# Optimization experiments

Hardware: AMD Instinct MI355X
Metric: run time of the kernel (lower is better)

Reference implementation:

```python
import jax, jax.numpy as jnp
import numpy as np

B = 256; NROIS = 200; IN = 200; HID = 128; L = 4; H = 8; RATIO = 0.5
K = int(np.ceil(RATIO * NROIS))        # SAGPooling top-k per graph = 100
N = B * NROIS                          # total nodes = 51200
DEG = 32; EPG = NROIS * DEG; E_EDGES = B * EPG  # 1,638,400 edges
EMB = HID * L                          # MHA embed dim = 512
DH = EMB // H

def _xavier(k, shape):
    fan_in, fan_out = shape[-2], shape[-1]
    lim = float(np.sqrt(6.0 / (fan_in + fan_out)))
    return jax.random.uniform(k, shape, jnp.float32, -lim, lim)

def setup_inputs() -> dict:
    key = jax.random.key(0)
    ks = jax.random.split(key, 16)
    x = jax.random.normal(ks[0], (N, IN), jnp.float32)
    # block-diagonal edge list: edges stay within each graph's node range
    src = jax.random.randint(ks[1], (E_EDGES,), 0, NROIS, jnp.int32)
    dst = jax.random.randint(ks[2], (E_EDGES,), 0, NROIS, jnp.int32)
    off = jnp.repeat(jnp.arange(B, dtype=jnp.int32) * NROIS, EPG)
    edge_index = jnp.stack([src + off, dst + off])
    edge_attr = jax.random.normal(ks[3], (E_EDGES,), jnp.float32)  # unused by the math
    batch = jnp.repeat(jnp.arange(B, dtype=jnp.int32), NROIS)
    return dict(
        x=x, edge_index=edge_index, edge_attr=edge_attr, batch=batch,
        gcn_w0=_xavier(ks[4], (IN, HID)),
        gcn_w=_xavier(ks[5], (L - 1, HID, HID)),
        gcn_b=jnp.zeros((L, HID), jnp.float32),
        lin1_w0=_xavier(ks[6], (IN + HID, HID)),
        lin1_w=_xavier(ks[7], (L - 1, 2 * HID, HID)),
        lin1_b=jnp.zeros((L, HID), jnp.float32),
        lin2_w=_xavier(ks[8], (L, HID, HID)),
        lin2_b=jnp.zeros((L, HID), jnp.float32),
        sag_w1=_xavier(ks[9], (HID, 1)),
        sag_w2=_xavier(ks[10], (HID, 1)),
        sag_b=jnp.zeros((1,), jnp.float32),
        mha_in_w=_xavier(ks[11], (3 * EMB, EMB)),
        mha_in_b=jnp.zeros((3 * EMB,), jnp.float32),
        mha_out_w=_xavier(ks[12], (EMB, EMB)),
        mha_out_b=jnp.zeros((EMB,), jnp.float32),
        fin_w=_xavier(ks[13], (EMB, HID)),
        fin_b=jnp.zeros((HID,), jnp.float32),
    )

def _gcn_conv(x, src, dst, W, b):
    xw = x @ W
    deg = jax.ops.segment_sum(jnp.ones_like(dst, jnp.float32), dst, num_segments=N) + 1.0
    dinv = jax.lax.rsqrt(deg)
    norm = dinv[src] * dinv[dst]                     # [E]
    agg = jax.ops.segment_sum(xw[src] * norm[:, None], dst, num_segments=N)
    agg = agg + xw * (dinv * dinv)[:, None]          # self-loop term
    return agg + b

def _gcblock(x, src, dst, gw, gb, l1w, l1b, l2w, l2b):
    x1 = jnp.tanh(_gcn_conv(x, src, dst, gw, gb))
    h = jnp.tanh(jnp.concatenate([x, x1], axis=1) @ l1w + l1b)
    return jnp.tanh(h @ l2w + l2b)

def _sag_pool_pad(z, src, dst, w1, w2, b):
    # SAGPooling score via PyG GraphConv (aggr='add'): lin_rel(sum_j x_j) + lin_root(x_i)
    neigh = jax.ops.segment_sum(z[src], dst, num_segments=N)
    score = (neigh @ w1)[:, 0] + b[0] + (z @ w2)[:, 0]        # [N]
    s3 = score.reshape(B, NROIS)
    vals, idx = jax.lax.top_k(s3, K)                           # [B,K]
    z3 = z.reshape(B, NROIS, HID)
    pooled = jnp.take_along_axis(z3, idx[:, :, None], axis=1) * jnp.tanh(vals)[:, :, None]
    zpad = jnp.zeros_like(z3).at[jnp.arange(B)[:, None], idx].set(pooled)
    return zpad.reshape(N, HID)

def reference(x, edge_index, edge_attr, batch,
              gcn_w0, gcn_w, gcn_b, lin1_w0, lin1_w, lin1_b, lin2_w, lin2_b,
              sag_w1, sag_w2, sag_b,
              mha_in_w, mha_in_b, mha_out_w, mha_out_b, fin_w, fin_b):
    src, dst = edge_index[0], edge_index[1]
    z = x
    pads = []
    for i in range(L):
        gw = gcn_w0 if i == 0 else gcn_w[i - 1]
        l1w = lin1_w0 if i == 0 else lin1_w[i - 1]
        z = _gcblock(z, src, dst, gw, gcn_b[i], l1w, lin1_b[i], lin2_w[i], lin2_b[i])
        pads.append(_sag_pool_pad(z, src, dst, sag_w1, sag_w2, sag_b))
    xc = jnp.concatenate(pads, axis=1).reshape(B, NROIS, EMB)   # [B,S,E]
    # MultiheadAttention (batch_first, eval mode -> no dropout)
    qkv = xc @ mha_in_w.T + mha_in_b                             # [B,S,3E]
    q, k, v = jnp.split(qkv, 3, axis=-1)
    def heads(t):
        return t.reshape(B, NROIS, H, DH).transpose(0, 2, 1, 3)  # [B,H,S,dh]
    q, k, v = heads(q), heads(k), heads(v)
    scores = jnp.einsum('bhqd,bhkd->bhqk', q, k) / np.sqrt(DH)
    attn = jax.nn.softmax(scores, axis=-1)                       # [B,H,S,S]
    o = jnp.einsum('bhqk,bhkd->bhqd', attn, v).transpose(0, 2, 1, 3).reshape(B, NROIS, EMB)
    o = o @ mha_out_w.T + mha_out_b
    attn_weights = attn.mean(axis=1)                             # avg over heads [B,S,S]
    # readout: global_mean_pool over each graph's nrois nodes
    pooled = o.mean(axis=1)                                      # [B,E]
    out = jnp.tanh(pooled @ fin_w + fin_b)                       # [B,HID]
    return out, attn_weights
```

## Files before the change

kernel.cpp:

```cpp
#include <hip/hip_runtime.h>
#include <hip/hip_fp16.h>


#define GB   256
#define SS   200
#define KIN  200
#define HD   128
#define NLAY 4
#define NHD  8
#define TOPK 100
#define NT   (GB * SS)
#define EPG_ 6400
#define NE_  (GB * EPG_)
#define EMB_ 512

typedef _Float16 half8 __attribute__((ext_vector_type(8)));
typedef _Float16 half4v __attribute__((ext_vector_type(4)));
typedef float floatx4 __attribute__((ext_vector_type(4)));

__global__ __launch_bounds__(256) void k_build_A(const int* __restrict__ src,
                                                 const int* __restrict__ dst,
                                                 float* __restrict__ A) {
  int e = blockIdx.x * 256 + threadIdx.x;
  if (e >= NE_) return;
  int d = dst[e], s = src[e];
  int b = d / SS;
  int dl = d - b * SS;
  int sl = s - b * SS;
  atomicAdd(&A[((size_t)b * SS + dl) * SS + sl], 1.0f);
}

__global__ __launch_bounds__(256) void k_dinv(const float* __restrict__ A,
                                              float* __restrict__ dinv) {
  int node = blockIdx.x * 4 + (threadIdx.x >> 6);
  int lane = threadIdx.x & 63;
  const float* r = A + (size_t)node * SS;
  float v = r[lane] + r[lane + 64] + r[lane + 128];
  if (lane < 8) v += r[lane + 192];
#pragma unroll
  for (int o = 32; o; o >>= 1) v += __shfl_xor(v, o);
  if (lane == 0) dinv[node] = rsqrtf(v + 1.0f);
}

__global__ __launch_bounds__(256) void k_prep_all(
    const float* __restrict__ gcn_w0, const float* __restrict__ gcn_w,
    const float* __restrict__ lin1_w0, const float* __restrict__ lin1_w,
    const float* __restrict__ lin2_w,
    __half* __restrict__ whi, __half* __restrict__ wlo) {
  const int mat = blockIdx.x >> 7;
  const int n   = blockIdx.x & 127;
  const int l = mat / 3, which = mat % 3;
  const float* src;
  int K, Kpad;
  if (which == 0) {
    K = l ? HD : KIN;  Kpad = l ? 128 : 256;
    src = l ? gcn_w + (size_t)(l - 1) * HD * HD : gcn_w0;
  } else if (which == 1) {
    K = l ? 2 * HD : KIN + HD;  Kpad = l ? 256 : 384;
    src = l ? lin1_w + (size_t)(l - 1) * 2 * HD * HD : lin1_w0;
  } else {
    K = HD;  Kpad = HD;
    src = lin2_w + (size_t)l * HD * HD;
  }
  int off = (l == 0) ? (which == 0 ? 0 : (which == 1 ? 32768 : 81920))
                     : 98304 + (l - 1) * 65536 +
                       (which == 0 ? 0 : (which == 1 ? 16384 : 49152));
  _Float16* wh = (_Float16*)whi + (size_t)off + (size_t)n * Kpad;
  _Float16* wl = (_Float16*)wlo + (size_t)off + (size_t)n * Kpad;
  for (int k = threadIdx.x; k < Kpad; k += 256) {
    float v = (k < K) ? src[(size_t)k * HD + n] : 0.f;
    _Float16 h = (_Float16)v;
    wh[k] = h;
    wl[k] = (_Float16)(v - (float)h);
  }
}

__global__ __launch_bounds__(256) void k_prep_w16(const float* __restrict__ W,
                                                  __half* __restrict__ W16) {
  int i = blockIdx.x * 256 + threadIdx.x;
  float4 v = reinterpret_cast<const float4*>(W)[i];
  half4v h = {(_Float16)v.x, (_Float16)v.y, (_Float16)v.z, (_Float16)v.w};
  *reinterpret_cast<half4v*>((_Float16*)W16 + (size_t)i * 4) = h;
}

__global__ __launch_bounds__(256) void k_node_mfma(
    const float* __restrict__ in1, int k1,
    const float* __restrict__ in2,
    const __half* __restrict__ Whi, const __half* __restrict__ Wlo,
    int Kpad,
    const float* __restrict__ bias,
    float* __restrict__ out, int doTanh) {
  const int m0 = blockIdx.x * 64;
  const int t = threadIdx.x;
  const int wave = t >> 6, lane = t & 63;
  const int col = lane & 15, quad = lane >> 4;
  const int wm = (wave & 1) * 32;
  const int wn = (wave >> 1) * 64;
  __shared__ __align__(16) _Float16 Ah[64][72];
  __shared__ __align__(16) _Float16 Al[64][72];
  floatx4 acc[2][4] = {};
  const int lr = t >> 2;
  const int lk = (t & 3) * 16;
  const _Float16* Wh = (const _Float16*)Whi;
  const _Float16* Wl = (const _Float16*)Wlo;

  for (int k0 = 0; k0 < Kpad; k0 += 64) {
    __syncthreads();
#pragma unroll
    for (int q = 0; q < 4; ++q) {
      int kg = k0 + lk + q * 4;
      float4 v = {0.f, 0.f, 0.f, 0.f};
      if (kg < k1)
        v = *reinterpret_cast<const float4*>(&in1[(size_t)(m0 + lr) * k1 + kg]);
      else if (in2 && kg < k1 + HD)
        v = *reinterpret_cast<const float4*>(&in2[(size_t)(m0 + lr) * HD + (kg - k1)]);
      half4v h = {(_Float16)v.x, (_Float16)v.y, (_Float16)v.z, (_Float16)v.w};
      half4v lo = {(_Float16)(v.x - (float)h.x), (_Float16)(v.y - (float)h.y),
                   (_Float16)(v.z - (float)h.z), (_Float16)(v.w - (float)h.w)};
      *reinterpret_cast<half4v*>(&Ah[lr][lk + q * 4]) = h;
      *reinterpret_cast<half4v*>(&Al[lr][lk + q * 4]) = lo;
    }
    __syncthreads();
#pragma unroll
    for (int ks = 0; ks < 2; ++ks) {
      half8 ah[2], al[2], bh[4], bl[4];
#pragma unroll
      for (int i = 0; i < 2; ++i) {
        ah[i] = *reinterpret_cast<const half8*>(&Ah[wm + i * 16 + col][ks * 32 + quad * 8]);
        al[i] = *reinterpret_cast<const half8*>(&Al[wm + i * 16 + col][ks * 32 + quad * 8]);
      }
#pragma unroll
      for (int j = 0; j < 4; ++j) {
        const size_t wo = (size_t)(wn + j * 16 + col) * Kpad + k0 + ks * 32 + quad * 8;
        bh[j] = *reinterpret_cast<const half8*>(Wh + wo);
        bl[j] = *reinterpret_cast<const half8*>(Wl + wo);
      }
#pragma unroll
      for (int i = 0; i < 2; ++i)
#pragma unroll
        for (int j = 0; j < 4; ++j) {
          acc[i][j] = __builtin_amdgcn_mfma_f32_16x16x32_f16(ah[i], bh[j], acc[i][j], 0, 0, 0);
          acc[i][j] = __builtin_amdgcn_mfma_f32_16x16x32_f16(ah[i], bl[j], acc[i][j], 0, 0, 0);
          acc[i][j] = __builtin_amdgcn_mfma_f32_16x16x32_f16(al[i], bh[j], acc[i][j], 0, 0, 0);
        }
    }
  }
#pragma unroll
  for (int j = 0; j < 4; ++j) {
    int n = wn + j * 16 + col;
    float bb = bias ? bias[n] : 0.f;
#pragma unroll
    for (int i = 0; i < 2; ++i) {
      int rbase = m0 + wm + i * 16 + quad * 4;
#pragma unroll
      for (int r = 0; r < 4; ++r) {
        float v = acc[i][j][r] + bb;
        if (doTanh) v = tanhf(v);
        out[(size_t)(rbase + r) * HD + n] = v;
      }
    }
  }
}

__global__ __launch_bounds__(256) void k_agg_mfma(
    const float* __restrict__ A, const float* __restrict__ dinv,
    const float* __restrict__ xw, const float* __restrict__ bias,
    float* __restrict__ out) {
  const int b    = blockIdx.x >> 1;
  const int row0 = (blockIdx.x & 1) * 128;
  const int t = threadIdx.x;
  const int wave = t >> 6, lane = t & 63;
  const int col = lane & 15, quad = lane >> 4;
  const int wm = (wave & 1) * 64, wn = (wave >> 1) * 64;
  __shared__ __align__(16) _Float16 Ah[128][72];
  __shared__ __align__(16) _Float16 Al[128][72];
  __shared__ __align__(16) _Float16 Bh[128][72];
  __shared__ __align__(16) _Float16 Bl[128][72];
  __shared__ float dvs[256];
  dvs[t] = (t < SS) ? dinv[b * SS + t] : 0.f;
  floatx4 acc[4][4] = {};
  const float* Ab  = A  + (size_t)b * SS * SS;
  const float* xwb = xw + (size_t)b * SS * HD;
  const int lr = t >> 1, lk = (t & 1) * 32;
  const int d = row0 + lr;
  __syncthreads();
  const float dvd = (d < SS) ? dvs[d] : 0.f;

  for (int k0 = 0; k0 < 256; k0 += 64) {
    __syncthreads();
#pragma unroll
    for (int q = 0; q < 8; ++q) {
      int s = k0 + lk + q * 4;
      float4 v = {0.f, 0.f, 0.f, 0.f};
      if (d < SS && s < SS)
        v = *reinterpret_cast<const float4*>(&Ab[(size_t)d * SS + s]);
      float e0 = (v.x + ((s + 0 == d) ? 1.f : 0.f)) * dvd * dvs[(s + 0) & 255];
      float e1 = (v.y + ((s + 1 == d) ? 1.f : 0.f)) * dvd * dvs[(s + 1) & 255];
      float e2 = (v.z + ((s + 2 == d) ? 1.f : 0.f)) * dvd * dvs[(s + 2) & 255];
      float e3 = (v.w + ((s + 3 == d) ? 1.f : 0.f)) * dvd * dvs[(s + 3) & 255];
      half4v h = {(_Float16)e0, (_Float16)e1, (_Float16)e2, (_Float16)e3};
      half4v lo = {(_Float16)(e0 - (float)h.x), (_Float16)(e1 - (float)h.y),
                   (_Float16)(e2 - (float)h.z), (_Float16)(e3 - (float)h.w)};
      *reinterpret_cast<half4v*>(&Ah[lr][lk + q * 4]) = h;
      *reinterpret_cast<half4v*>(&Al[lr][lk + q * 4]) = lo;
    }
#pragma unroll
    for (int p = 0; p < 8; ++p) {
      int idx = t + p * 256;
      int c4 = idx & 31, ss = idx >> 5;
      int s = k0 + ss;
      float4 v = {0.f, 0.f, 0.f, 0.f};
      if (s < SS)
        v = *reinterpret_cast<const float4*>(&xwb[(size_t)s * HD + c4 * 4]);
      int ssx = ss ^ ((c4 & 7) << 3);
      float e[4] = {v.x, v.y, v.z, v.w};
#pragma unroll
      for (int j = 0; j < 4; ++j) {
        _Float16 h = (_Float16)e[j];
        Bh[c4 * 4 + j][ssx] = h;
        Bl[c4 * 4 + j][ssx] = (_Float16)(e[j] - (float)h);
      }
    }
    __syncthreads();
#pragma unroll
    for (int ks = 0; ks < 2; ++ks) {
      half8 ah[4], al[4], bh[4], bl[4];
#pragma unroll
      for (int i = 0; i < 4; ++i) {
        ah[i] = *reinterpret_cast<const half8*>(&Ah[wm + i * 16 + col][ks * 32 + quad * 8]);
        al[i] = *reinterpret_cast<const half8*>(&Al[wm + i * 16 + col][ks * 32 + quad * 8]);
      }
#pragma unroll
      for (int j = 0; j < 4; ++j) {
        int n = wn + j * 16 + col;
        int koff = (ks * 32 + quad * 8) ^ (((n >> 2) & 7) << 3);
        bh[j] = *reinterpret_cast<const half8*>(&Bh[n][koff]);
        bl[j] = *reinterpret_cast<const half8*>(&Bl[n][koff]);
      }
#pragma unroll
      for (int i = 0; i < 4; ++i)
#pragma unroll
        for (int j = 0; j < 4; ++j) {
          acc[i][j] = __builtin_amdgcn_mfma_f32_16x16x32_f16(ah[i], bh[j], acc[i][j], 0, 0, 0);
          acc[i][j] = __builtin_amdgcn_mfma_f32_16x16x32_f16(ah[i], bl[j], acc[i][j], 0, 0, 0);
          acc[i][j] = __builtin_amdgcn_mfma_f32_16x16x32_f16(al[i], bh[j], acc[i][j], 0, 0, 0);
        }
    }
  }
#pragma unroll
  for (int j = 0; j < 4; ++j) {
    int n = wn + j * 16 + col;
    float bb = bias[n];
#pragma unroll
    for (int i = 0; i < 4; ++i) {
      int rbase = row0 + wm + i * 16 + quad * 4;
#pragma unroll
      for (int r = 0; r < 4; ++r) {
        int row = rbase + r;
        if (row < SS)
          out[((size_t)b * SS + row) * HD + n] = tanhf(acc[i][j][r] + bb);
      }
    }
  }
}

__global__ __launch_bounds__(256) void k_sag(
    const float* __restrict__ z, const float* __restrict__ A,
    const float* __restrict__ w1, const float* __restrict__ w2,
    const float* __restrict__ sb,
    __half* __restrict__ xch, __half* __restrict__ xcl, int layer) {
  const int b = blockIdx.x, t = threadIdx.x;
  __shared__ float w1s[HD], w2s[HD];
  __shared__ float zw1[SS], sc[SS], fac[SS];
  if (t < HD) { w1s[t] = w1[t]; w2s[t] = w2[t]; }
  __syncthreads();
  float a2 = 0.f;
  if (t < SS) {
    const float4* zr = reinterpret_cast<const float4*>(&z[((size_t)b * SS + t) * HD]);
    float a1 = 0.f;
#pragma unroll
    for (int q = 0; q < HD / 4; ++q) {
      float4 v = zr[q];
      a1 += v.x * w1s[4 * q] + v.y * w1s[4 * q + 1] + v.z * w1s[4 * q + 2] + v.w * w1s[4 * q + 3];
      a2 += v.x * w2s[4 * q] + v.y * w2s[4 * q + 1] + v.z * w2s[4 * q + 2] + v.w * w2s[4 * q + 3];
    }
    zw1[t] = a1;
  }
  __syncthreads();
  if (t < SS) {
    float s = sb[0] + a2;
    const float4* ar = reinterpret_cast<const float4*>(&A[((size_t)b * SS + t) * SS]);
#pragma unroll 5
    for (int q = 0; q < SS / 4; ++q) {
      float4 v = ar[q];
      s += v.x * zw1[4 * q] + v.y * zw1[4 * q + 1] + v.z * zw1[4 * q + 2] + v.w * zw1[4 * q + 3];
    }
    sc[t] = s;
  }
  __syncthreads();
  if (t < SS) {
    float si = sc[t];
    int cnt = 0;
    for (int j = 0; j < SS; ++j) {
      float sj = sc[j];
      cnt += (sj > si || (sj == si && j < t)) ? 1 : 0;
    }
    fac[t] = (cnt < TOPK) ? tanhf(si) : 0.f;
  }
  __syncthreads();
  _Float16* xh = (_Float16*)xch;
  _Float16* xl = (_Float16*)xcl;
  for (int idx = t; idx < SS * HD; idx += 256) {
    int row = idx >> 7, c = idx & 127;
    float v = fac[row] * z[((size_t)b * SS + row) * HD + c];
    _Float16 h = (_Float16)v;
    size_t o = ((size_t)b * SS + row) * EMB_ + layer * HD + c;
    xh[o] = h;
    xl[o] = (_Float16)(v - (float)h);
  }
}

__global__ __launch_bounds__(256) void k_proj(
    const __half* __restrict__ xch, const __half* __restrict__ Win16,
    const float* __restrict__ bin, __half* __restrict__ QKh) {
  const int wg = (blockIdx.x & 7) * 400 + (blockIdx.x >> 3);
  const int bm = wg >> 3;
  const int bn = wg & 7;
  const int m0 = bm * 128, n0 = bn * 128;
  const int t = threadIdx.x;
  const int wave = t >> 6, lane = t & 63;
  const int col = lane & 15, quad = lane >> 4;
  const int wm = (wave & 1) * 64;
  const int wn = (wave >> 1) * 64;
  floatx4 acc[4][4] = {};
  const _Float16* X = (const _Float16*)xch;
  const _Float16* W = (const _Float16*)Win16;
  const _Float16* xa[4];
  const _Float16* wb[4];
#pragma unroll
  for (int i = 0; i < 4; ++i)
    xa[i] = X + (size_t)(m0 + wm + i * 16 + col) * EMB_ + quad * 8;
#pragma unroll
  for (int j = 0; j < 4; ++j)
    wb[j] = W + (size_t)(n0 + wn + j * 16 + col) * EMB_ + quad * 8;

#pragma unroll 4
  for (int k0 = 0; k0 < EMB_; k0 += 32) {
    half8 af[4], bf[4];
#pragma unroll
    for (int i = 0; i < 4; ++i) af[i] = *reinterpret_cast<const half8*>(xa[i] + k0);
#pragma unroll
    for (int j = 0; j < 4; ++j) bf[j] = *reinterpret_cast<const half8*>(wb[j] + k0);
#pragma unroll
    for (int i = 0; i < 4; ++i)
#pragma unroll
      for (int j = 0; j < 4; ++j)
        acc[i][j] = __builtin_amdgcn_mfma_f32_16x16x32_f16(af[i], bf[j], acc[i][j], 0, 0, 0);
  }
#pragma unroll
  for (int j = 0; j < 4; ++j) {
    int c = n0 + wn + j * 16 + col;
    float bb = bin[c];
#pragma unroll
    for (int i = 0; i < 4; ++i) {
      int rbase = m0 + wm + i * 16 + quad * 4;
#pragma unroll
      for (int r = 0; r < 4; ++r)
        QKh[(size_t)(rbase + r) * 1024 + c] = __float2half(acc[i][j][r] + bb);
    }
  }
}

__global__ __launch_bounds__(256) void k_attn(
    const __half* __restrict__ QKh,
    float* __restrict__ cpbuf,
    float* __restrict__ attn) {
  const int bx = (blockIdx.x & 7) * 416 + (blockIdx.x >> 3);
  const int b  = bx / 13;
  const int it = bx % 13;
  const int i0 = it * 16;
  const int rows = (SS - i0 >= 16) ? 16 : (SS - i0);
  const int t    = threadIdx.x;
  const int wave = t >> 6;
  const int lane = t & 63;
  const int col  = lane & 15;
  const int quad = lane >> 4;

  __shared__ __align__(16) float Ss[16][212];

  float am[13];
  int   soff[13];
  int   kmax = 0;
#pragma unroll
  for (int k = 0; k < 13; ++k) {
    int idx = t + (k << 8);
    am[k] = 0.f;
    if (idx < rows * 200) {
      int i = idx / 200;
      soff[k] = idx + 12 * i;
      kmax = k + 1;
    } else soff[k] = 0;
  }

  const _Float16* Qbase = (const _Float16*)QKh + (size_t)b * SS * 1024;
  const _Float16* qrow = Qbase + (size_t)(i0 + col) * 1024 + quad * 8;
  const _Float16* krow[4];
#pragma unroll
  for (int m = 0; m < 4; ++m) {
    int jt = wave + m * 4;
    krow[m] = Qbase + (size_t)(jt * 16 + col) * 1024 + 512 + quad * 8;
  }

  for (int h = 0; h < NHD; ++h) {
    const int hoff = h * 64;
    half8 a0 = *reinterpret_cast<const half8*>(qrow + hoff);
    half8 a1 = *reinterpret_cast<const half8*>(qrow + hoff + 32);
#pragma unroll
    for (int m = 0; m < 4; ++m) {
      int jt = wave + m * 4;
      if (jt < 13) {
        half8 b0 = *reinterpret_cast<const half8*>(krow[m] + hoff);
        half8 b1 = *reinterpret_cast<const half8*>(krow[m] + hoff + 32);
        floatx4 acc = {0.f, 0.f, 0.f, 0.f};
        acc = __builtin_amdgcn_mfma_f32_16x16x32_f16(a0, b0, acc, 0, 0, 0);
        acc = __builtin_amdgcn_mfma_f32_16x16x32_f16(a1, b1, acc, 0, 0, 0);
#pragma unroll
        for (int r = 0; r < 4; ++r)
          Ss[quad * 4 + r][jt * 16 + col] = acc[r] * 0.125f;
      }
    }
    __syncthreads();
#pragma unroll
    for (int ri = 0; ri < 4; ++ri) {
      int r = wave * 4 + ri;
      if (r < rows) {
        float* srow = &Ss[r][0];
        float s0 = srow[lane], s1 = srow[lane + 64], s2 = srow[lane + 128];
        float s3 = (lane < 8) ? srow[lane + 192] : -1e30f;
        float mx = fmaxf(fmaxf(s0, s1), fmaxf(s2, s3));
#pragma unroll
        for (int o = 32; o; o >>= 1) mx = fmaxf(mx, __shfl_xor(mx, o));
        float e0 = __expf(s0 - mx), e1 = __expf(s1 - mx), e2 = __expf(s2 - mx);
        float e3 = (lane < 8) ? __expf(s3 - mx) : 0.f;
        float sum = e0 + e1 + e2 + e3;
#pragma unroll
        for (int o = 32; o; o >>= 1) sum += __shfl_xor(sum, o);
        float rl = 1.0f / sum;
        srow[lane] = e0 * rl; srow[lane + 64] = e1 * rl; srow[lane + 128] = e2 * rl;
        if (lane < 8) srow[lane + 192] = e3 * rl;
      }
    }
    __syncthreads();
    const float* sflat = &Ss[0][0];
#pragma unroll
    for (int k = 0; k < 13; ++k)
      if (k < kmax) am[k] += sflat[soff[k]] * 0.125f;
    if (t < SS) {
      float s = 0.f;
      for (int i = 0; i < rows; ++i) s += Ss[i][t];
      atomicAdd(&cpbuf[((size_t)b * NHD + h) * SS + t], s);
    }
    __syncthreads();
  }
  float* abase = &attn[((size_t)b * SS + i0) * SS];
#pragma unroll
  for (int k = 0; k < 13; ++k)
    if (k < kmax) abase[t + (k << 8)] = am[k];
}

__global__ __launch_bounds__(256) void k_pool(
    const __half* __restrict__ xch, const __half* __restrict__ xcl,
    const float* __restrict__ cpbuf,
    const float* __restrict__ Win, const float* __restrict__ bin,
    float* __restrict__ pooled) {
  const int b = blockIdx.x, t = threadIdx.x;
  __shared__ float cps[NHD][SS];
  __shared__ float tvs[NHD][EMB_];
  for (int idx = t; idx < NHD * SS; idx += 256) {
    int h = idx / SS, j = idx - h * SS;
    cps[h][j] = cpbuf[((size_t)b * NHD + h) * SS + j];
  }
  __syncthreads();
  const _Float16* xh = (const _Float16*)xch + (size_t)b * SS * EMB_;
  const _Float16* xl = (const _Float16*)xcl + (size_t)b * SS * EMB_;
  float a0[NHD] = {0.f}, a1[NHD] = {0.f};
  for (int j = 0; j < SS; ++j) {
    float x0 = (float)xh[(size_t)j * EMB_ + t] + (float)xl[(size_t)j * EMB_ + t];
    float x1 = (float)xh[(size_t)j * EMB_ + t + 256] + (float)xl[(size_t)j * EMB_ + t + 256];
#pragma unroll
    for (int h = 0; h < NHD; ++h) {
      float c = cps[h][j];
      a0[h] += c * x0; a1[h] += c * x1;
    }
  }
#pragma unroll
  for (int h = 0; h < NHD; ++h) { tvs[h][t] = a0[h]; tvs[h][t + 256] = a1[h]; }
  __syncthreads();
  const int wv = t >> 6, lane = t & 63;
  for (int e = wv; e < EMB_; e += 4) {
    int h = e >> 6;
    const float* wr = Win + (size_t)(2 * EMB_ + e) * EMB_;
    float s = 0.f;
#pragma unroll
    for (int q = 0; q < 8; ++q) s += wr[lane + q * 64] * tvs[h][lane + q * 64];
#pragma unroll
    for (int o = 32; o; o >>= 1) s += __shfl_xor(s, o);
    if (lane == 0) pooled[(size_t)b * EMB_ + e] = bin[2 * EMB_ + e] * (float)SS + s;
  }
}

__global__ __launch_bounds__(256) void k_final(
    const float* __restrict__ pooled, const float* __restrict__ Wout,
    const float* __restrict__ bout, const float* __restrict__ finw,
    const float* __restrict__ finb, float* __restrict__ out) {
  const int b = blockIdx.x, t = threadIdx.x;
  __shared__ float pl[EMB_], po[EMB_];
  for (int k = t; k < EMB_; k += 256) pl[k] = pooled[(size_t)b * EMB_ + k] * (1.0f / (float)SS);
  __syncthreads();
  for (int e = t; e < EMB_; e += 256) {
    const float* wr = &Wout[(size_t)e * EMB_];
    float a = bout[e];
    for (int k = 0; k < EMB_; ++k) a += wr[k] * pl[k];
    po[e] = a;
  }
  __syncthreads();
  if (t < HD) {
    float a = finb[t];
    for (int e = 0; e < EMB_; ++e) a += po[e] * finw[(size_t)e * HD + t];
    out[(size_t)b * HD + t] = tanhf(a);
  }
}

extern "C" void kernel_launch(void* const* d_in, const int* in_sizes, int n_in,
                              void* d_out, int out_size, void* d_ws, size_t ws_size,
                              hipStream_t stream) {
  const float* x         = (const float*)d_in[0];
  const int*   ei        = (const int*)d_in[1];
  const float* gcn_w0    = (const float*)d_in[4];
  const float* gcn_w     = (const float*)d_in[5];
  const float* gcn_b     = (const float*)d_in[6];
  const float* lin1_w0   = (const float*)d_in[7];
  const float* lin1_w    = (const float*)d_in[8];
  const float* lin1_b    = (const float*)d_in[9];
  const float* lin2_w    = (const float*)d_in[10];
  const float* lin2_b    = (const float*)d_in[11];
  const float* sag_w1    = (const float*)d_in[12];
  const float* sag_w2    = (const float*)d_in[13];
  const float* sag_b     = (const float*)d_in[14];
  const float* mha_in_w  = (const float*)d_in[15];
  const float* mha_in_b  = (const float*)d_in[16];
  const float* mha_out_w = (const float*)d_in[17];
  const float* mha_out_b = (const float*)d_in[18];
  const float* fin_w     = (const float*)d_in[19];
  const float* fin_b     = (const float*)d_in[20];

  float* ws     = (float*)d_ws;
  float* dinv   = ws;
  float* Araw   = dinv + NT;
  float* buf0   = Araw + (size_t)GB * SS * SS;
  float* buf1   = buf0 + (size_t)NT * HD;
  float* zbuf   = buf1 + (size_t)NT * HD;
  float* xcf    = zbuf + (size_t)NT * HD;
  __half* xch   = (__half*)xcf;
  __half* xcl   = xch + (size_t)NT * EMB_;
  float* pooled = xcf + (size_t)NT * EMB_;
  __half* QKh  = (__half*)Araw;
  float* cpbuf = Araw + 26214400;

  float* outp = (float*)d_out;
  float* attn = outp + (size_t)GB * HD;

  __half* whi   = (__half*)attn;
  __half* wlo   = whi + 294912;
  __half* Win16 = wlo + 294912;

  hipMemsetAsync(Araw, 0, (size_t)GB * SS * SS * sizeof(float), stream);

  k_prep_all<<<12 * 128, 256, 0, stream>>>(gcn_w0, gcn_w, lin1_w0, lin1_w, lin2_w, whi, wlo);
  k_prep_w16<<<512, 256, 0, stream>>>(mha_in_w, Win16);
  k_build_A<<<NE_ / 256, 256, 0, stream>>>(ei, ei + NE_, Araw);
  k_dinv<<<NT / 4, 256, 0, stream>>>(Araw, dinv);

  static const int KPg[4]  = {256, 128, 128, 128};
  static const int KP1[4]  = {384, 256, 256, 256};
  static const int OFFg[4] = {0, 98304, 163840, 229376};
  static const int OFF1[4] = {32768, 114688, 180224, 245760};
  static const int OFF2[4] = {81920, 147456, 212992, 278528};

  for (int l = 0; l < NLAY; ++l) {
    const float* zin = (l == 0) ? x : zbuf;
    int k1 = (l == 0) ? KIN : HD;
    k_node_mfma<<<NT / 64, 256, 0, stream>>>(zin, k1, nullptr,
                                             whi + OFFg[l], wlo + OFFg[l], KPg[l],
                                             nullptr, buf0, 0);
    k_agg_mfma<<<GB * 2, 256, 0, stream>>>(Araw, dinv, buf0, gcn_b + l * HD, buf1);
    k_node_mfma<<<NT / 64, 256, 0, stream>>>(zin, k1, buf1,
                                             whi + OFF1[l], wlo + OFF1[l], KP1[l],
                                             lin1_b + l * HD, buf0, 1);
    k_node_mfma<<<NT / 64, 256, 0, stream>>>(buf0, HD, nullptr,
                                             whi + OFF2[l], wlo + OFF2[l], HD,
                                             lin2_b + l * HD, zbuf, 1);
    k_sag<<<GB, 256, 0, stream>>>(zbuf, Araw, sag_w1, sag_w2, sag_b, xch, xcl, l);
  }

  hipMemsetAsync(cpbuf, 0, (size_t)GB * NHD * SS * sizeof(float), stream);
  k_proj<<<(NT / 128) * 8, 256, 0, stream>>>(xch, Win16, mha_in_b, QKh);
  k_attn<<<GB * 13, 256, 0, stream>>>(QKh, cpbuf, attn);
  k_pool<<<GB, 256, 0, stream>>>(xch, xcl, cpbuf, mha_in_w, mha_in_b, pooled);
  k_final<<<GB, 256, 0, stream>>>(pooled, mha_out_w, mha_out_b, fin_w, fin_b, outp);
}
```

Measured before the change: 1.575 ms.

## Stage QKV projection tiles in LDS via direct global-to-LDS loads with swizzle

The QK projection GEMM previously had each wave load its MFMA fragments straight from global memory, so the same A and B rows were fetched redundantly across waves. Each block now stages 128x64 half tiles of A and B in shared memory using global_load_lds with an XOR swizzle, then reads fragments from LDS. This is meant to cut global traffic and improve coalescing, at the cost of two barriers per k-step and no double buffering.

Measured after the change: 1.450 ms. -7.9%, faster.

```diff
diff --git a/kernel.cpp b/kernel.cpp
--- a/kernel.cpp
+++ b/kernel.cpp
@@ -332,30 +332,51 @@
   const int col = lane & 15, quad = lane >> 4;
   const int wm = (wave & 1) * 64;
   const int wn = (wave >> 1) * 64;
+  __shared__ __align__(16) _Float16 As[128][64];
+  __shared__ __align__(16) _Float16 Bs[128][64];
   floatx4 acc[4][4] = {};
   const _Float16* X = (const _Float16*)xch;
   const _Float16* W = (const _Float16*)Win16;
-  const _Float16* xa[4];
-  const _Float16* wb[4];
-#pragma unroll
-  for (int i = 0; i < 4; ++i)
-    xa[i] = X + (size_t)(m0 + wm + i * 16 + col) * EMB_ + quad * 8;
-#pragma unroll
-  for (int j = 0; j < 4; ++j)
-    wb[j] = W + (size_t)(n0 + wn + j * 16 + col) * EMB_ + quad * 8;
-
-#pragma unroll 4
-  for (int k0 = 0; k0 < EMB_; k0 += 32) {
-    half8 af[4], bf[4];
-#pragma unroll
-    for (int i = 0; i < 4; ++i) af[i] = *reinterpret_cast<const half8*>(xa[i] + k0);
-#pragma unroll
-    for (int j = 0; j < 4; ++j) bf[j] = *reinterpret_cast<const half8*>(wb[j] + k0);
-#pragma unroll
-    for (int i = 0; i < 4; ++i)
+
+  const int srow = lane >> 3;
+  const int sch  = (lane & 7) ^ srow;
+  const int arow = wave * 8 + srow;
+  const int fsw = col & 7;
+
+  for (int k0 = 0; k0 < EMB_; k0 += 64) {
+#pragma unroll
+    for (int q = 0; q < 4; ++q) {
+      const _Float16* ga = X + (size_t)(m0 + q * 32 + arow) * EMB_ + k0 + sch * 8;
+      __builtin_amdgcn_global_load_lds(
+          (const __attribute__((address_space(1))) void*)ga,
+          (__attribute__((address_space(3))) void*)((char*)&As[0][0] + q * 4096 + wave * 1024),
+          16, 0, 0);
+      const _Float16* gb = W + (size_t)(n0 + q * 32 + arow) * EMB_ + k0 + sch * 8;
+      __builtin_amdgcn_global_load_lds(
+          (const __attribute__((address_space(1))) void*)gb,
+          (__attribute__((address_space(3))) void*)((char*)&Bs[0][0] + q * 4096 + wave * 1024),
+          16, 0, 0);
+    }
+    __syncthreads();
+#pragma unroll
+    for (int ks = 0; ks < 2; ++ks) {
+      const int ch = (ks * 4 + quad) ^ fsw;
+      half8 af[4], bf[4];
+#pragma unroll
+      for (int i = 0; i < 4; ++i)
+        af[i] = *reinterpret_cast<const half8*>(
+            (const char*)&As[0][0] + (wm + i * 16 + col) * 128 + ch * 16);
 #pragma unroll
       for (int j = 0; j < 4; ++j)
-        acc[i][j] = __builtin_amdgcn_mfma_f32_16x16x32_f16(af[i], bf[j], acc[i][j], 0, 0, 0);
+        bf[j] = *reinterpret_cast<const half8*>(
+            (const char*)&Bs[0][0] + (wn + j * 16 + col) * 128 + ch * 16);
+#pragma unroll
+      for (int i = 0; i < 4; ++i)
+#pragma unroll
+        for (int j = 0; j < 4; ++j)
+          acc[i][j] = __builtin_amdgcn_mfma_f32_16x16x32_f16(af[i], bf[j], acc[i][j], 0, 0, 0);
+    }
+    __syncthreads();
   }
 #pragma unroll
   for (int j = 0; j < 4; ++j) {
```
